# Kernel tuning notes

Measured on AMD Instinct MI355X. Metric: run time of the kernel, lower is better.

Reference implementation:

```python
import jax, jax.numpy as jnp
import numpy as np

N = 100000      # nodes
F_IN = 512      # input features
HID = 256       # hidden
C = 50          # classes
E = 1_600_000   # edges
K = 10          # APPNP iterations
ALPHA = 1.0     # teleport prob (as hard-coded in source: APPNP(10, 1))


def setup_inputs() -> dict:
    key = jax.random.key(0)
    k1, k2, k3, k4, k5, k6 = jax.random.split(key, 6)
    x = jax.random.normal(k1, (N, F_IN), dtype=jnp.float32)
    edge_index = jax.random.randint(k2, (2, E), 0, N, dtype=jnp.int32)
    # Linear params (torch nn.Linear default init scale ~ 1/sqrt(fan_in))
    W1 = jax.random.uniform(k3, (F_IN, HID), jnp.float32, -1.0, 1.0) / np.sqrt(F_IN)
    b1 = jax.random.uniform(k4, (HID,), jnp.float32, -1.0, 1.0) / np.sqrt(F_IN)
    W2 = jax.random.uniform(k5, (HID, C), jnp.float32, -1.0, 1.0) / np.sqrt(HID)
    b2 = jax.random.uniform(k6, (C,), jnp.float32, -1.0, 1.0) / np.sqrt(HID)
    return {"x": x, "edge_index": edge_index, "W1": W1, "b1": b1, "W2": W2, "b2": b2}


def _appnp(h, edge_index):
    # gcn_norm with self-loops: A_hat = D^{-1/2} (A + I) D^{-1/2}
    loops = jnp.arange(N, dtype=edge_index.dtype)
    src = jnp.concatenate([edge_index[0], loops])  # message sources
    dst = jnp.concatenate([edge_index[1], loops])  # aggregation targets
    deg = jax.ops.segment_sum(jnp.ones_like(dst, dtype=h.dtype), dst, num_segments=N)
    dinv = jnp.where(deg > 0, jax.lax.rsqrt(deg), 0.0)
    norm = (dinv[src] * dinv[dst])[:, None]  # [E+N, 1]

    def step(z, _):
        agg = jax.ops.segment_sum(norm * z[src], dst, num_segments=N)  # [N, C]
        z = (1.0 - ALPHA) * agg + ALPHA * h
        return z, None

    z, _ = jax.lax.scan(step, h, None, length=K)
    return z


def reference(x, edge_index, W1, b1, W2, b2):
    # eval mode: dropout is identity
    h = jax.nn.relu(x @ W1 + b1)   # [N, HID]
    h = h @ W2 + b2                # [N, C]
    z = _appnp(h, edge_index)      # K-step personalized-pagerank propagation
    return jax.nn.log_softmax(z, axis=1)
```

## Files before the change

### kernel.cpp

```cpp
#include <hip/hip_runtime.h>
#include <cstdint>
#include <cstddef>

#define NROWS 100000
#define FIN 512
#define HIDDEN 256
#define NCLS 50

typedef __attribute__((ext_vector_type(8))) short s16x8;
typedef __attribute__((ext_vector_type(4))) float f32x4;

__device__ __forceinline__ unsigned short f2bf(float f) {
  unsigned int u = __float_as_uint(f);
  u += 0x7fffu + ((u >> 16) & 1u);
  return (unsigned short)(u >> 16);
}

__device__ __forceinline__ unsigned int cvt_pk_bf16(float lo, float hi) {
  unsigned int r;
  asm("v_cvt_pk_bf16_f32 %0, %1, %2" : "=v"(r) : "v"(lo), "v"(hi));
  return r;
}

__device__ __forceinline__ void gload_lds16(const void* g, void* l) {
  __builtin_amdgcn_global_load_lds(
      (const __attribute__((address_space(1))) void*)g,
      (__attribute__((address_space(3))) void*)l, 16, 0, 0);
}

__device__ __forceinline__ f32x4 mfma_bf16(s16x8 a, s16x8 b, f32x4 c) {
  return __builtin_amdgcn_mfma_f32_16x16x32_bf16(a, b, c, 0, 0, 0);
}

__global__ __launch_bounds__(256) void prep_kernel(
    const float* __restrict__ W1, const float* __restrict__ W2,
    unsigned short* __restrict__ w1t, unsigned short* __restrict__ w2t) {
  __shared__ float tile[64][65];
  const int b = blockIdx.x, t = threadIdx.x;
  if (b < 32) {
    const int k0 = (b >> 2) * 64, n0 = (b & 3) * 64;
    const int rq = t >> 6, col = t & 63;
#pragma unroll
    for (int i = 0; i < 16; ++i) {
      int row = i * 4 + rq;
      tile[row][col] = W1[(size_t)(k0 + row) * HIDDEN + n0 + col];
    }
    __syncthreads();
#pragma unroll
    for (int i = 0; i < 16; ++i) {
      int n = i * 4 + rq;
      w1t[(size_t)(n0 + n) * FIN + k0 + col] = f2bf(tile[col][n]);
    }
  } else {
    const int b2i = b - 32;
#pragma unroll
    for (int i = 0; i < 16; ++i) {
      int idx = t + i * 256;
      int c = idx >> 6;
      int k = b2i * 64 + (idx & 63);
      float v = (c < NCLS) ? W2[(size_t)k * NCLS + c] : 0.0f;
      w2t[(size_t)c * HIDDEN + k] = f2bf(v);
    }
  }
}

__global__ __launch_bounds__(512, 4) void fused_kernel(
    const float* __restrict__ x, const unsigned short* __restrict__ w1t,
    const unsigned short* __restrict__ w2t, const float* __restrict__ b1,
    const float* __restrict__ b2, float* __restrict__ out) {
  __shared__ char smem[65536];
  float* const Abase = (float*)smem;
  unsigned short* const Bbase = (unsigned short*)(smem + 32768);

  const int t = threadIdx.x;
  const int lane = t & 63, wid = t >> 6;
  const int q = lane & 15, half = lane >> 4;
  const int wr = wid >> 1, wc = wid & 1;
  const int bm = blockIdx.x;

  auto stage_A = [&](float* buf, int k0) {
#pragma unroll
    for (int i = 0; i < 2; ++i) {
      int c = t + i * 512;
      int row = c >> 3, s = c & 7;
      int grow = bm * 128 + row;
      if (grow > NROWS - 1) grow = NROWS - 1;
      gload_lds16(x + (size_t)grow * FIN + k0 + ((s ^ (row & 7)) << 2),
                  buf + c * 4);
    }
  };
  auto stage_B = [&](unsigned short* buf, int k0) {
#pragma unroll
    for (int i = 0; i < 2; ++i) {
      int c = t + i * 512;
      int col = c >> 2, s = c & 3;
      gload_lds16(w1t + (size_t)col * FIN + k0 + ((s ^ ((col >> 2) & 3)) << 3),
                  buf + c * 8);
    }
  };

  f32x4 acc[2][8];
  const f32x4 z4 = {0.f, 0.f, 0.f, 0.f};
#pragma unroll
  for (int m = 0; m < 2; ++m)
#pragma unroll
    for (int n = 0; n < 8; ++n) acc[m][n] = z4;

  stage_A(Abase, 0);
  stage_B(Bbase, 0);
  __syncthreads();

  for (int ks = 0; ks < 16; ++ks) {
    const int cur = ks & 1;
    float* Ac = Abase + cur * 4096;
    unsigned short* Bc = Bbase + cur * 8192;
    if (ks < 15) {
      stage_A(Abase + (cur ^ 1) * 4096, (ks + 1) * 32);
      stage_B(Bbase + (cur ^ 1) * 8192, (ks + 1) * 32);
    }

    s16x8 af[2];
#pragma unroll
    for (int m = 0; m < 2; ++m) {
      const int row = wr * 32 + m * 16 + q;
      const int cb = row * 8;
      f32x4 lo = *(const f32x4*)(Ac + (cb + ((half * 2) ^ (q & 7))) * 4);
      f32x4 hi = *(const f32x4*)(Ac + (cb + ((half * 2 + 1) ^ (q & 7))) * 4);
      union { unsigned int u[4]; s16x8 v; } cvu;
      cvu.u[0] = cvt_pk_bf16(lo[0], lo[1]);
      cvu.u[1] = cvt_pk_bf16(lo[2], lo[3]);
      cvu.u[2] = cvt_pk_bf16(hi[0], hi[1]);
      cvu.u[3] = cvt_pk_bf16(hi[2], hi[3]);
      af[m] = cvu.v;
    }

#pragma unroll
    for (int n = 0; n < 8; ++n) {
      const int col = wc * 128 + n * 16 + q;
      s16x8 bf = *(const s16x8*)(Bc + col * 32 + ((half ^ ((q >> 2) & 3)) << 3));
      acc[0][n] = mfma_bf16(af[0], bf, acc[0][n]);
      acc[1][n] = mfma_bf16(af[1], bf, acc[1][n]);
    }
    __syncthreads();
  }

  unsigned short* const hls = (unsigned short*)smem;
  unsigned short* const wls = Bbase;
  const int p_of_wave = wid >> 2;

#pragma unroll
  for (int i = 0; i < 4; ++i) {
    int c = t + i * 512;
    int row = c >> 5, s = c & 31;
    gload_lds16(w2t + (size_t)row * HIDDEN + ((s ^ (row & 7)) << 3), wls + c * 8);
  }

  auto write_h = [&]() {
#pragma unroll
    for (int n = 0; n < 8; ++n) {
      const int col = wc * 128 + n * 16 + q;
      const float bias = b1[col];
      const int chs = col & 7;
#pragma unroll
      for (int m = 0; m < 2; ++m) {
        const int rl0 = (wr & 1) * 32 + m * 16 + half * 4;
#pragma unroll
        for (int r = 0; r < 4; ++r) {
          const int rl = rl0 + r;
          float v = fmaxf(acc[m][n][r] + bias, 0.0f);
          const int ch = (col >> 3) ^ (rl & 7);
          hls[rl * 256 + ch * 8 + chs] = f2bf(v);
        }
      }
    }
  };

  auto gemm2_pass = [&](int p) {
    f32x4 acc2[4];
#pragma unroll
    for (int n = 0; n < 4; ++n) acc2[n] = z4;
    const int arl = (wid & 3) * 16 + q;
#pragma unroll
    for (int ks = 0; ks < HIDDEN; ks += 32) {
      const int g = (ks >> 3) + half;
      s16x8 a2 = *(const s16x8*)(hls + arl * 256 + ((g ^ (arl & 7)) << 3));
#pragma unroll
      for (int n = 0; n < 4; ++n) {
        const int c = n * 16 + q;
        s16x8 b2f = *(const s16x8*)(wls + c * 256 + ((g ^ (c & 7)) << 3));
        acc2[n] = mfma_bf16(a2, b2f, acc2[n]);
      }
    }
    float bias2[4];
#pragma unroll
    for (int n = 0; n < 4; ++n) {
      const int c = n * 16 + q;
      bias2[n] = (c < NCLS) ? b2[c] : 0.0f;
    }
#pragma unroll
    for (int r = 0; r < 4; ++r) {
      float vals[4];
      float mx = -1e30f;
#pragma unroll
      for (int n = 0; n < 4; ++n) {
        const int c = n * 16 + q;
        float v = acc2[n][r] + bias2[n];
        vals[n] = v;
        if (c < NCLS) mx = fmaxf(mx, v);
      }
      for (int off = 8; off >= 1; off >>= 1)
        mx = fmaxf(mx, __shfl_xor(mx, off, 64));
      float s = 0.f;
#pragma unroll
      for (int n = 0; n < 4; ++n) {
        const int c = n * 16 + q;
        if (c < NCLS) s += __expf(vals[n] - mx);
      }
      for (int off = 8; off >= 1; off >>= 1) s += __shfl_xor(s, off, 64);
      const float lz = __logf(s);
      const int rowg = bm * 128 + p * 64 + (wid & 3) * 16 + half * 4 + r;
      if (rowg < NROWS) {
#pragma unroll
        for (int n = 0; n < 4; ++n) {
          const int c = n * 16 + q;
          if (c < NCLS) out[(size_t)rowg * NCLS + c] = vals[n] - mx - lz;
        }
      }
    }
  };

  if (p_of_wave == 0) write_h();
  __syncthreads();
  if (p_of_wave == 0) gemm2_pass(0);
  __syncthreads();
  if (p_of_wave == 1) write_h();
  __syncthreads();
  if (p_of_wave == 1) gemm2_pass(1);
}

extern "C" void kernel_launch(void* const* d_in, const int* in_sizes, int n_in,
                              void* d_out, int out_size, void* d_ws, size_t ws_size,
                              hipStream_t stream) {
  const float* x  = (const float*)d_in[0];
  const float* W1 = (const float*)d_in[2];
  const float* b1 = (const float*)d_in[3];
  const float* W2 = (const float*)d_in[4];
  const float* b2 = (const float*)d_in[5];
  float* out = (float*)d_out;

  char* ws = (char*)d_ws;
  unsigned short* w1t = (unsigned short*)(ws);
  unsigned short* w2t = (unsigned short*)(ws + 262144);

  prep_kernel<<<36, 256, 0, stream>>>(W1, W2, w1t, w2t);
  fused_kernel<<<(NROWS + 127) / 128, 512, 0, stream>>>(x, w1t, w2t, b1, b2, out);
}
```

Before: 66.36 us.

## Switch to 32x32x16 MFMA, convert x to bf16 in registers before LDS

Both GEMMs now use 32x32x16 bf16 MFMA tiles instead of 16x16x32, with a new 2x4 wave layout and new swizzled LDS layouts. The x tile is loaded into registers, converted to bf16 and written to LDS, replacing the fp32 async copy to LDS. This halves LDS footprint and removes repeated per-wave conversion. The second GEMM splits classes across two waves and merges their log-sum-exp partials through LDS. The cost is more barriers and register pressure, and the x loads now go through registers rather than direct async LDS copies, which may expose global latency.

Result: slower. 91.07 us (+37.2%).

```diff
diff --git a/kernel.cpp b/kernel.cpp
--- a/kernel.cpp
+++ b/kernel.cpp
@@ -9,6 +9,7 @@
 
 typedef __attribute__((ext_vector_type(8))) short s16x8;
 typedef __attribute__((ext_vector_type(4))) float f32x4;
+typedef __attribute__((ext_vector_type(16))) float f32x16;
 
 __device__ __forceinline__ unsigned short f2bf(float f) {
   unsigned int u = __float_as_uint(f);
@@ -28,8 +29,8 @@
       (__attribute__((address_space(3))) void*)l, 16, 0, 0);
 }
 
-__device__ __forceinline__ f32x4 mfma_bf16(s16x8 a, s16x8 b, f32x4 c) {
-  return __builtin_amdgcn_mfma_f32_16x16x32_bf16(a, b, c, 0, 0, 0);
+__device__ __forceinline__ f32x16 mfma32(s16x8 a, s16x8 b, f32x16 c) {
+  return __builtin_amdgcn_mfma_f32_32x32x16_bf16(a, b, c, 0, 0, 0);
 }
 
 __global__ __launch_bounds__(256) void prep_kernel(
@@ -69,173 +70,198 @@
     const unsigned short* __restrict__ w2t, const float* __restrict__ b1,
     const float* __restrict__ b2, float* __restrict__ out) {
   __shared__ char smem[65536];
-  float* const Abase = (float*)smem;
-  unsigned short* const Bbase = (unsigned short*)(smem + 32768);
 
   const int t = threadIdx.x;
   const int lane = t & 63, wid = t >> 6;
-  const int q = lane & 15, half = lane >> 4;
-  const int wr = wid >> 1, wc = wid & 1;
+  const int l31 = lane & 31, l5 = lane >> 5;
+  const int wrM = wid >> 2, wcN = wid & 3;
   const int bm = blockIdx.x;
 
-  auto stage_A = [&](float* buf, int k0) {
-#pragma unroll
-    for (int i = 0; i < 2; ++i) {
-      int c = t + i * 512;
-      int row = c >> 3, s = c & 7;
-      int grow = bm * 128 + row;
-      if (grow > NROWS - 1) grow = NROWS - 1;
-      gload_lds16(x + (size_t)grow * FIN + k0 + ((s ^ (row & 7)) << 2),
-                  buf + c * 4);
-    }
-  };
-  auto stage_B = [&](unsigned short* buf, int k0) {
-#pragma unroll
-    for (int i = 0; i < 2; ++i) {
-      int c = t + i * 512;
-      int col = c >> 2, s = c & 3;
-      gload_lds16(w1t + (size_t)col * FIN + k0 + ((s ^ ((col >> 2) & 3)) << 3),
-                  buf + c * 8);
-    }
-  };
-
-  f32x4 acc[2][8];
-  const f32x4 z4 = {0.f, 0.f, 0.f, 0.f};
-#pragma unroll
-  for (int m = 0; m < 2; ++m)
-#pragma unroll
-    for (int n = 0; n < 8; ++n) acc[m][n] = z4;
-
-  stage_A(Abase, 0);
-  stage_B(Bbase, 0);
+  const int arow = t >> 2, as4 = t & 3;
+  int growA = bm * 128 + arow;
+  if (growA > NROWS - 1) growA = NROWS - 1;
+  const float* const asrc = x + (size_t)growA * FIN + as4 * 8;
+  char* const aw_dst0 = smem + (arow >> 6) * 4096 + (as4 >> 1) * 2048 +
+                        ((arow >> 5) & 1) * 1024 +
+                        ((((as4 & 1) << 5) + (arow & 31)) << 4);
+
+  const unsigned short* bsrc[2];
+  char* bdst[2];
+#pragma unroll
+  for (int i = 0; i < 2; ++i) {
+    const int c = t + i * 512;
+    const int colB = c >> 2, sB = c & 3;
+    const int sg = sB ^ (((colB >> 1) & 1) << 1);
+    bsrc[i] = w1t + (size_t)colB * FIN + sg * 8;
+    bdst[i] = smem + 16384 + c * 16;
+  }
+  auto stage_B = [&](int buf, int k0) {
+#pragma unroll
+    for (int i = 0; i < 2; ++i) gload_lds16(bsrc[i] + k0, bdst[i] + buf * 16384);
+  };
+
+  int aro[2][2], bro[2][2];
+#pragma unroll
+  for (int ksub = 0; ksub < 2; ++ksub) {
+#pragma unroll
+    for (int mfi = 0; mfi < 2; ++mfi)
+      aro[ksub][mfi] = wrM * 4096 + ksub * 2048 + mfi * 1024 + lane * 16;
+#pragma unroll
+    for (int nfi = 0; nfi < 2; ++nfi) {
+      const int colR = wcN * 64 + nfi * 32 + l31;
+      const int slotR = ((ksub << 1) + l5) ^ (((l31 >> 1) & 1) << 1);
+      bro[ksub][nfi] = 16384 + colR * 64 + slotR * 16;
+    }
+  }
+
+  f32x16 acc[2][2];
+#pragma unroll
+  for (int i = 0; i < 2; ++i)
+#pragma unroll
+    for (int j = 0; j < 2; ++j)
+#pragma unroll
+      for (int r = 0; r < 16; ++r) acc[i][j][r] = 0.0f;
+
+  {
+    float4 a0 = ((const float4*)asrc)[0];
+    float4 a1 = ((const float4*)asrc)[1];
+    stage_B(0, 0);
+    unsigned int u0 = cvt_pk_bf16(a0.x, a0.y), u1 = cvt_pk_bf16(a0.z, a0.w);
+    unsigned int u2 = cvt_pk_bf16(a1.x, a1.y), u3 = cvt_pk_bf16(a1.z, a1.w);
+    *(uint4*)aw_dst0 = make_uint4(u0, u1, u2, u3);
+  }
   __syncthreads();
 
   for (int ks = 0; ks < 16; ++ks) {
     const int cur = ks & 1;
-    float* Ac = Abase + cur * 4096;
-    unsigned short* Bc = Bbase + cur * 8192;
+    float4 na0, na1;
     if (ks < 15) {
-      stage_A(Abase + (cur ^ 1) * 4096, (ks + 1) * 32);
-      stage_B(Bbase + (cur ^ 1) * 8192, (ks + 1) * 32);
-    }
-
-    s16x8 af[2];
-#pragma unroll
-    for (int m = 0; m < 2; ++m) {
-      const int row = wr * 32 + m * 16 + q;
-      const int cb = row * 8;
-      f32x4 lo = *(const f32x4*)(Ac + (cb + ((half * 2) ^ (q & 7))) * 4);
-      f32x4 hi = *(const f32x4*)(Ac + (cb + ((half * 2 + 1) ^ (q & 7))) * 4);
-      union { unsigned int u[4]; s16x8 v; } cvu;
-      cvu.u[0] = cvt_pk_bf16(lo[0], lo[1]);
-      cvu.u[1] = cvt_pk_bf16(lo[2], lo[3]);
-      cvu.u[2] = cvt_pk_bf16(hi[0], hi[1]);
-      cvu.u[3] = cvt_pk_bf16(hi[2], hi[3]);
-      af[m] = cvu.v;
-    }
-
-#pragma unroll
-    for (int n = 0; n < 8; ++n) {
-      const int col = wc * 128 + n * 16 + q;
-      s16x8 bf = *(const s16x8*)(Bc + col * 32 + ((half ^ ((q >> 2) & 3)) << 3));
-      acc[0][n] = mfma_bf16(af[0], bf, acc[0][n]);
-      acc[1][n] = mfma_bf16(af[1], bf, acc[1][n]);
+      na0 = ((const float4*)(asrc + (ks + 1) * 32))[0];
+      na1 = ((const float4*)(asrc + (ks + 1) * 32))[1];
+      stage_B(cur ^ 1, (ks + 1) * 32);
+    }
+    const int ab = cur * 8192, bb = cur * 16384;
+    s16x8 af[2][2], bfv[2][2];
+#pragma unroll
+    for (int ksub = 0; ksub < 2; ++ksub) {
+#pragma unroll
+      for (int mfi = 0; mfi < 2; ++mfi)
+        af[ksub][mfi] = *(const s16x8*)(smem + ab + aro[ksub][mfi]);
+#pragma unroll
+      for (int nfi = 0; nfi < 2; ++nfi)
+        bfv[ksub][nfi] = *(const s16x8*)(smem + bb + bro[ksub][nfi]);
+    }
+#pragma unroll
+    for (int ksub = 0; ksub < 2; ++ksub)
+#pragma unroll
+      for (int mfi = 0; mfi < 2; ++mfi)
+#pragma unroll
+        for (int nfi = 0; nfi < 2; ++nfi)
+          acc[mfi][nfi] = mfma32(af[ksub][mfi], bfv[ksub][nfi], acc[mfi][nfi]);
+    if (ks < 15) {
+      unsigned int u0 = cvt_pk_bf16(na0.x, na0.y), u1 = cvt_pk_bf16(na0.z, na0.w);
+      unsigned int u2 = cvt_pk_bf16(na1.x, na1.y), u3 = cvt_pk_bf16(na1.z, na1.w);
+      *(uint4*)(aw_dst0 + (cur ^ 1) * 8192) = make_uint4(u0, u1, u2, u3);
     }
     __syncthreads();
   }
 
-  unsigned short* const hls = (unsigned short*)smem;
-  unsigned short* const wls = Bbase;
-  const int p_of_wave = wid >> 2;
-
 #pragma unroll
   for (int i = 0; i < 4; ++i) {
-    int c = t + i * 512;
-    int row = c >> 5, s = c & 31;
-    gload_lds16(w2t + (size_t)row * HIDDEN + ((s ^ (row & 7)) << 3), wls + c * 8);
+    const int c = t + i * 512;
+    const int rw = c >> 5, sl = c & 31;
+    gload_lds16(w2t + (size_t)rw * 256 + (sl ^ (rw & 7)) * 8, smem + 32768 + c * 16);
   }
 
   auto write_h = [&]() {
-#pragma unroll
-    for (int n = 0; n < 8; ++n) {
-      const int col = wc * 128 + n * 16 + q;
-      const float bias = b1[col];
-      const int chs = col & 7;
-#pragma unroll
-      for (int m = 0; m < 2; ++m) {
-        const int rl0 = (wr & 1) * 32 + m * 16 + half * 4;
-#pragma unroll
-        for (int r = 0; r < 4; ++r) {
-          const int rl = rl0 + r;
-          float v = fmaxf(acc[m][n][r] + bias, 0.0f);
-          const int ch = (col >> 3) ^ (rl & 7);
-          hls[rl * 256 + ch * 8 + chs] = f2bf(v);
+    float b1c[2];
+#pragma unroll
+    for (int nfi = 0; nfi < 2; ++nfi) b1c[nfi] = b1[wcN * 64 + nfi * 32 + l31];
+#pragma unroll
+    for (int nfi = 0; nfi < 2; ++nfi) {
+      const int col = wcN * 64 + nfi * 32 + l31;
+      const int cbase = ((col >> 4) << 10) + (((col >> 3) & 1) << 9) + ((col & 7) << 1);
+      const int x2 = (col >> 3) & 3;
+#pragma unroll
+      for (int mfi = 0; mfi < 2; ++mfi) {
+        char* const hb = smem + mfi * 16384 + cbase;
+#pragma unroll
+        for (int r = 0; r < 16; ++r) {
+          const int crow = (r & 3) + ((r >> 2) << 3) + (l5 << 2);
+          float v = fmaxf(acc[mfi][nfi][r] + b1c[nfi], 0.0f);
+          *(unsigned short*)(hb + ((crow ^ x2) << 4)) = (unsigned short)cvt_pk_bf16(v, v);
         }
       }
     }
   };
 
-  auto gemm2_pass = [&](int p) {
-    f32x4 acc2[4];
-#pragma unroll
-    for (int n = 0; n < 4; ++n) acc2[n] = z4;
-    const int arl = (wid & 3) * 16 + q;
-#pragma unroll
-    for (int ks = 0; ks < HIDDEN; ks += 32) {
-      const int g = (ks >> 3) + half;
-      s16x8 a2 = *(const s16x8*)(hls + arl * 256 + ((g ^ (arl & 7)) << 3));
-#pragma unroll
-      for (int n = 0; n < 4; ++n) {
-        const int c = n * 16 + q;
-        s16x8 b2f = *(const s16x8*)(wls + c * 256 + ((g ^ (c & 7)) << 3));
-        acc2[n] = mfma_bf16(a2, b2f, acc2[n]);
-      }
-    }
-    float bias2[4];
-#pragma unroll
-    for (int n = 0; n < 4; ++n) {
-      const int c = n * 16 + q;
-      bias2[n] = (c < NCLS) ? b2[c] : 0.0f;
-    }
-#pragma unroll
-    for (int r = 0; r < 4; ++r) {
-      float vals[4];
-      float mx = -1e30f;
-#pragma unroll
-      for (int n = 0; n < 4; ++n) {
-        const int c = n * 16 + q;
-        float v = acc2[n][r] + bias2[n];
-        vals[n] = v;
-        if (c < NCLS) mx = fmaxf(mx, v);
-      }
-      for (int off = 8; off >= 1; off >>= 1)
-        mx = fmaxf(mx, __shfl_xor(mx, off, 64));
-      float s = 0.f;
-#pragma unroll
-      for (int n = 0; n < 4; ++n) {
-        const int c = n * 16 + q;
-        if (c < NCLS) s += __expf(vals[n] - mx);
-      }
-      for (int off = 8; off >= 1; off >>= 1) s += __shfl_xor(s, off, 64);
-      const float lz = __logf(s);
-      const int rowg = bm * 128 + p * 64 + (wid & 3) * 16 + half * 4 + r;
-      if (rowg < NROWS) {
-#pragma unroll
-        for (int n = 0; n < 4; ++n) {
-          const int c = n * 16 + q;
-          if (c < NCLS) out[(size_t)rowg * NCLS + c] = vals[n] - mx - lz;
-        }
-      }
-    }
-  };
-
-  if (p_of_wave == 0) write_h();
-  __syncthreads();
-  if (p_of_wave == 0) gemm2_pass(0);
-  __syncthreads();
-  if (p_of_wave == 1) write_h();
-  __syncthreads();
-  if (p_of_wave == 1) gemm2_pass(1);
+  const int local = wid & 3;
+  const int rg = local & 1, cgw = local >> 1;
+  const int classc = cgw * 32 + l31;
+  const bool valid = classc < NCLS;
+  const float bias2v = valid ? b2[classc] : 0.0f;
+  f32x16 acc2;
+#pragma unroll
+  for (int r = 0; r < 16; ++r) acc2[r] = 0.0f;
+
+  auto gemm2_kloop = [&]() {
+#pragma unroll
+    for (int ksub = 0; ksub < 16; ++ksub) {
+      const int k8a = (ksub << 1) + l5;
+      s16x8 a2 = *(const s16x8*)(smem + rg * 16384 + (ksub << 10) +
+                                 ((lane ^ (k8a & 3)) << 4));
+      s16x8 b2f = *(const s16x8*)(smem + 32768 + classc * 512 +
+                                  ((k8a ^ (classc & 7)) << 4));
+      acc2 = mfma32(a2, b2f, acc2);
+    }
+  };
+
+  auto lse_partial = [&]() {
+#pragma unroll
+    for (int r = 0; r < 16; ++r) {
+      const int crow = (r & 3) + ((r >> 2) << 3) + (l5 << 2);
+      float v = valid ? (acc2[r] + bias2v) : -3.0e38f;
+      float m = v;
+#pragma unroll
+      for (int off = 16; off >= 1; off >>= 1) m = fmaxf(m, __shfl_xor(m, off, 64));
+      float sE = valid ? __expf(v - m) : 0.0f;
+#pragma unroll
+      for (int off = 16; off >= 1; off >>= 1) sE += __shfl_xor(sE, off, 64);
+      if (l31 == 0)
+        *(float2*)(smem + cgw * 512 + (rg * 32 + crow) * 8) = make_float2(m, sE);
+    }
+  };
+
+  auto lse_store = [&](int p) {
+#pragma unroll
+    for (int r = 0; r < 16; ++r) {
+      const int crow = (r & 3) + ((r >> 2) << 3) + (l5 << 2);
+      const int rowid = rg * 32 + crow;
+      float2 e0 = *(const float2*)(smem + cgw * 512 + rowid * 8);
+      float2 e1 = *(const float2*)(smem + (cgw ^ 1) * 512 + rowid * 8);
+      float M = fmaxf(e0.x, e1.x);
+      float lz = __logf(e0.y * __expf(e0.x - M) + e1.y * __expf(e1.x - M));
+      const int grow = bm * 128 + p * 64 + rowid;
+      if (valid && grow < NROWS)
+        out[(size_t)grow * NCLS + classc] = acc2[r] + bias2v - M - lz;
+    }
+  };
+
+  if (wrM == 0) write_h();
+  __syncthreads();
+  if (wrM == 0) gemm2_kloop();
+  __syncthreads();
+  if (wrM == 0) lse_partial();
+  __syncthreads();
+  if (wrM == 0) lse_store(0);
+  __syncthreads();
+  if (wrM == 1) write_h();
+  __syncthreads();
+  if (wrM == 1) gemm2_kloop();
+  __syncthreads();
+  if (wrM == 1) lse_partial();
+  __syncthreads();
+  if (wrM == 1) lse_store(1);
 }
 
 extern "C" void kernel_launch(void* const* d_in, const int* in_sizes, int n_in,
```
